# Kernel optimization log

Hardware: AMD Instinct MI355X
Metric: run time of the kernel (lower is better)

## Reference

```python
import jax, jax.numpy as jnp
import numpy as np


def setup_inputs() -> dict:
    key = jax.random.key(0)
    ks = jax.random.split(key, 7)
    B, T, I, H, O = 256, 500, 256, 512, 100
    std = 1.0 / np.sqrt(H)
    u = lambda k, shape: jax.random.uniform(k, shape, jnp.float32, -std, std)
    return {
        "x": jax.random.normal(ks[0], (B, T, I), jnp.float32),
        "Wx": u(ks[1], (4 * H, I)),
        "bx": u(ks[2], (4 * H,)),
        "Wh": u(ks[3], (4 * H, H)),
        "bh": u(ks[4], (4 * H,)),
        "Wfc": jax.random.normal(ks[5], (O, H), jnp.float32) * 0.02,
        "bfc": jnp.zeros((O,), jnp.float32),
    }


def reference(x, Wx, bx, Wh, bh, Wfc, bfc):
    B, T, I = x.shape
    H = Wh.shape[1]
    # Precompute input projections for all timesteps: [T, B, 4H]
    xg = jnp.einsum("bti,gi->tbg", x, Wx) + bx + bh

    def step(carry, xg_t):
        h, c = carry
        gates = xg_t + h @ Wh.T  # [B, 4H]
        i, f, g, o = jnp.split(gates, 4, axis=1)
        i = jax.nn.sigmoid(i)
        f = jax.nn.sigmoid(f)
        g = jnp.tanh(g)
        o = jax.nn.sigmoid(o)
        c = c * f + i * g
        h = o * jnp.tanh(c)
        return (h, c), None

    h0 = jnp.zeros((B, H), x.dtype)
    c0 = jnp.zeros((B, H), x.dtype)
    (hT, _), _ = jax.lax.scan(step, (h0, c0), xg)
    return hT @ Wfc.T + bfc  # [B, O]
```

## Files before the change

### kernel.cpp

```cpp
#include <hip/hip_runtime.h>
#include <hip/hip_bf16.h>

#define B_ 256
#define T_ 500
#define I_ 256
#define H_ 512
#define G_ 2048
#define O_ 100

typedef __attribute__((ext_vector_type(8))) short short8;
typedef __attribute__((ext_vector_type(4))) float f32x4;

#define WHB_OFF 0u
#define WXB_OFF (G_*H_*2u)
#define BSUM_OFF (WXB_OFF + G_*I_*2u)
#define H0_OFF  (BSUM_OFF + G_*4u)
#define H1_OFF  (H0_OFF + B_*H_*2u)
#define C_OFF   (H1_OFF + B_*H_*2u)
#define HT_OFF  (C_OFF + B_*H_*4u)

__device__ __forceinline__ float sigm(float v) { return 1.0f / (1.0f + __expf(-v)); }
__device__ __forceinline__ float tanh_fast(float v) { return 2.0f / (1.0f + __expf(-2.0f * v)) - 1.0f; }

__device__ __forceinline__ short f2bf_s(float f) {
  union { __hip_bfloat16 h; unsigned short u; } cv;
  cv.h = __float2bfloat16(f);
  return (short)cv.u;
}

__global__ void cast_kernel(const float* __restrict__ Wh, const float* __restrict__ Wx,
                            const float* __restrict__ bx, const float* __restrict__ bh,
                            short* __restrict__ Whb, short* __restrict__ Wxb,
                            float* __restrict__ bsum) {
  int idx = blockIdx.x * 256 + threadIdx.x;
  if (idx < G_ * H_) Whb[idx] = f2bf_s(Wh[idx]);
  if (idx < G_ * I_) Wxb[idx] = f2bf_s(Wx[idx]);
  if (idx < G_)      bsum[idx] = bx[idx] + bh[idx];
}

__global__ __launch_bounds__(128)
void lstm_step(const float* __restrict__ x, int t,
               const short* __restrict__ Whb, const short* __restrict__ Wxb,
               const float* __restrict__ bsum,
               const short* __restrict__ h_in,
               unsigned short* __restrict__ h_out,
               float* __restrict__ c,
               float* __restrict__ hT) {
  const int lane = threadIdx.x & 63;
  const int w    = threadIdx.x >> 6;
  const int r    = lane & 15;
  const int ko   = (lane >> 4) << 3;
  const int brow = blockIdx.y * 32 + w * 16;
  const int cbase = blockIdx.x * 16;

  f32x4 acc[4];
  #pragma unroll
  for (int q = 0; q < 4; ++q) { acc[q][0] = 0.f; acc[q][1] = 0.f; acc[q][2] = 0.f; acc[q][3] = 0.f; }

  const short* ha = h_in + (size_t)(brow + r) * H_ + ko;
  #pragma unroll 4
  for (int kk = 0; kk < H_; kk += 32) {
    short8 a = *reinterpret_cast<const short8*>(ha + kk);
    #pragma unroll
    for (int q = 0; q < 4; ++q) {
      const short* bp = Whb + (size_t)(q * H_ + cbase + r) * H_ + kk + ko;
      short8 b = *reinterpret_cast<const short8*>(bp);
      acc[q] = __builtin_amdgcn_mfma_f32_16x16x32_bf16(a, b, acc[q], 0, 0, 0);
    }
  }

  const float* xrow = x + ((size_t)(brow + r) * T_ + t) * I_ + ko;
  #pragma unroll 2
  for (int kk = 0; kk < I_; kk += 32) {
    float4 x0 = *reinterpret_cast<const float4*>(xrow + kk);
    float4 x1 = *reinterpret_cast<const float4*>(xrow + kk + 4);
    short8 a;
    a[0] = f2bf_s(x0.x); a[1] = f2bf_s(x0.y); a[2] = f2bf_s(x0.z); a[3] = f2bf_s(x0.w);
    a[4] = f2bf_s(x1.x); a[5] = f2bf_s(x1.y); a[6] = f2bf_s(x1.z); a[7] = f2bf_s(x1.w);
    #pragma unroll
    for (int q = 0; q < 4; ++q) {
      const short* bp = Wxb + (size_t)(q * H_ + cbase + r) * I_ + kk + ko;
      short8 b = *reinterpret_cast<const short8*>(bp);
      acc[q] = __builtin_amdgcn_mfma_f32_16x16x32_bf16(a, b, acc[q], 0, 0, 0);
    }
  }

  #pragma unroll
  for (int q = 0; q < 4; ++q) {
    float bb = bsum[q * H_ + cbase + r];
    acc[q][0] += bb; acc[q][1] += bb; acc[q][2] += bb; acc[q][3] += bb;
  }

  const int cell = cbase + r;
  #pragma unroll
  for (int j = 0; j < 4; ++j) {
    const int row = brow + ((lane >> 4) << 2) + j;
    const size_t ci = (size_t)row * H_ + cell;
    float ig = sigm(acc[0][j]);
    float fg = sigm(acc[1][j]);
    float gg = tanh_fast(acc[2][j]);
    float og = sigm(acc[3][j]);
    float cn = c[ci] * fg + ig * gg;
    c[ci] = cn;
    float hn = og * tanh_fast(cn);
    h_out[ci] = (unsigned short)f2bf_s(hn);
    if (hT) hT[ci] = hn;
  }
}

__global__ __launch_bounds__(128)
void fc_kernel(const float* __restrict__ hT, const float* __restrict__ Wfc,
               const float* __restrict__ bfc, float* __restrict__ out) {
  int b = blockIdx.x;
  int o = threadIdx.x;
  if (o >= O_) return;
  const float* hr = hT + (size_t)b * H_;
  const float* wr = Wfc + (size_t)o * H_;
  float s = 0.f;
  #pragma unroll 4
  for (int k = 0; k < H_; k += 4) {
    float4 hv = *reinterpret_cast<const float4*>(hr + k);
    float4 wv = *reinterpret_cast<const float4*>(wr + k);
    s += hv.x * wv.x + hv.y * wv.y + hv.z * wv.z + hv.w * wv.w;
  }
  out[b * O_ + o] = s + bfc[o];
}

extern "C" void kernel_launch(void* const* d_in, const int* in_sizes, int n_in,
                              void* d_out, int out_size, void* d_ws, size_t ws_size,
                              hipStream_t stream) {
  const float* x   = (const float*)d_in[0];
  const float* Wx  = (const float*)d_in[1];
  const float* bx  = (const float*)d_in[2];
  const float* Wh  = (const float*)d_in[3];
  const float* bh  = (const float*)d_in[4];
  const float* Wfc = (const float*)d_in[5];
  const float* bfc = (const float*)d_in[6];
  float* out = (float*)d_out;
  char* ws = (char*)d_ws;

  short* Whb  = (short*)(ws + WHB_OFF);
  short* Wxb  = (short*)(ws + WXB_OFF);
  float* bsum = (float*)(ws + BSUM_OFF);
  short* h0   = (short*)(ws + H0_OFF);
  short* h1   = (short*)(ws + H1_OFF);
  float* cbuf = (float*)(ws + C_OFF);
  float* hT   = (float*)(ws + HT_OFF);

  hipMemsetAsync(ws + H0_OFF, 0, B_ * H_ * 2, stream);
  hipMemsetAsync(ws + C_OFF,  0, B_ * H_ * 4, stream);

  cast_kernel<<<(G_ * H_ + 255) / 256, 256, 0, stream>>>(Wh, Wx, bx, bh, Whb, Wxb, bsum);

  for (int t = 0; t < T_; ++t) {
    const short* hin = (t & 1) ? h1 : h0;
    unsigned short* hout = (unsigned short*)((t & 1) ? h0 : h1);
    lstm_step<<<dim3(32, 8), 128, 0, stream>>>(x, t, Whb, Wxb, bsum, hin, hout, cbuf,
                                               (t == T_ - 1) ? hT : nullptr);
  }

  fc_kernel<<<B_, 128, 0, stream>>>(hT, Wfc, bfc, out);
}
```

Before: 6.285 ms.

## Replace per-timestep launches with persistent cooperative LSTM kernel and group barriers

```diff
diff --git a/kernel.cpp b/kernel.cpp
--- a/kernel.cpp
+++ b/kernel.cpp
@@ -8,24 +8,159 @@
 #define G_ 2048
 #define O_ 100
 
+#define NGRP 8
+#define GRP_BLKS 32
+#define CNT_STRIDE 32
+
 typedef __attribute__((ext_vector_type(8))) short short8;
 typedef __attribute__((ext_vector_type(4))) float f32x4;
 
-#define WHB_OFF 0u
-#define WXB_OFF (G_*H_*2u)
+#define WHB_OFF  0u
+#define WXB_OFF  (G_*H_*2u)
 #define BSUM_OFF (WXB_OFF + G_*I_*2u)
-#define H0_OFF  (BSUM_OFF + G_*4u)
-#define H1_OFF  (H0_OFF + B_*H_*2u)
-#define C_OFF   (H1_OFF + B_*H_*2u)
-#define HT_OFF  (C_OFF + B_*H_*4u)
+#define H0_OFF   (BSUM_OFF + G_*4u)
+#define H1_OFF   (H0_OFF + B_*H_*2u)
+#define C_OFF    (H1_OFF + B_*H_*2u)
+#define HT_OFF   (C_OFF + B_*H_*4u)
+#define CNT_OFF  (HT_OFF + B_*H_*4u)
 
 __device__ __forceinline__ float sigm(float v) { return 1.0f / (1.0f + __expf(-v)); }
 __device__ __forceinline__ float tanh_fast(float v) { return 2.0f / (1.0f + __expf(-2.0f * v)) - 1.0f; }
 
-__device__ __forceinline__ short f2bf_s(float f) {
+__device__ __forceinline__ short f2bf(float f) {
   union { __hip_bfloat16 h; unsigned short u; } cv;
   cv.h = __float2bfloat16(f);
   return (short)cv.u;
+}
+__device__ __forceinline__ short8 cvt8(float4 a, float4 b) {
+  short8 s;
+  s[0]=f2bf(a.x); s[1]=f2bf(a.y); s[2]=f2bf(a.z); s[3]=f2bf(a.w);
+  s[4]=f2bf(b.x); s[5]=f2bf(b.y); s[6]=f2bf(b.z); s[7]=f2bf(b.w);
+  return s;
+}
+
+__global__ __launch_bounds__(128, 1)
+void lstm_persist(const float* __restrict__ x, const float* __restrict__ Wx,
+                  const float* __restrict__ bx, const float* __restrict__ Wh,
+                  const float* __restrict__ bh,
+                  unsigned short* __restrict__ hbuf0, unsigned short* __restrict__ hbuf1,
+                  unsigned int* __restrict__ cnt)
+{
+  __shared__ short whlds[32768];
+  char* ldsb = (char*)whlds;
+
+  const int tid = threadIdx.x;
+  const int l   = tid & 63;
+  const int w   = tid >> 6;
+  const int g   = blockIdx.x & 7;
+  const int cc  = blockIdx.x >> 3;
+  const int rbase = g * 32 + w * 16;
+  const int cbase = cc * 16;
+  const int r   = l & 15;
+  const int u   = l >> 4;
+  const int rx  = (r & 7) << 4;
+
+  {
+    const int gc = tid >> 1;
+    const int kh = (tid & 1) * 256;
+    const int q = gc >> 4, li = gc & 15;
+    const float* src = Wh + ((size_t)(q * H_ + cbase + li)) * H_ + kh;
+    const int rowb = gc * (H_ * 2);
+    const int wxz = (gc & 7) << 4;
+    for (int k = 0; k < 256; k += 8) {
+      float4 f0 = *(const float4*)(src + k);
+      float4 f1 = *(const float4*)(src + k + 4);
+      int byte = (rowb + (kh + k) * 2) ^ wxz;
+      *(short8*)(ldsb + byte) = cvt8(f0, f1);
+    }
+  }
+
+  short8 wxr[4][8];
+  #pragma unroll
+  for (int q = 0; q < 4; ++q)
+    #pragma unroll
+    for (int kc = 0; kc < 8; ++kc) {
+      const float* p = Wx + ((size_t)(q * H_ + cbase + r)) * I_ + kc * 32 + u * 8;
+      wxr[q][kc] = cvt8(*(const float4*)p, *(const float4*)(p + 4));
+    }
+
+  float bsum[4];
+  #pragma unroll
+  for (int q = 0; q < 4; ++q)
+    bsum[q] = bx[q * H_ + cbase + r] + bh[q * H_ + cbase + r];
+
+  float creg[4] = {0.f, 0.f, 0.f, 0.f};
+
+  __syncthreads();
+
+  short8 xf[8];
+  #pragma unroll
+  for (int kc = 0; kc < 8; ++kc) {
+    const float* p = x + ((size_t)(rbase + r) * T_ + 0) * I_ + kc * 32 + u * 8;
+    xf[kc] = cvt8(*(const float4*)p, *(const float4*)(p + 4));
+  }
+
+  unsigned int* mycnt = cnt + g * CNT_STRIDE;
+
+  for (int t = 0; t < T_; ++t) {
+    const unsigned short* hin = (t & 1) ? hbuf1 : hbuf0;
+    unsigned short* hout      = (t & 1) ? hbuf0 : hbuf1;
+
+    f32x4 acc[4];
+    #pragma unroll
+    for (int q = 0; q < 4; ++q) acc[q] = (f32x4){0.f, 0.f, 0.f, 0.f};
+
+    #pragma unroll
+    for (int kc = 0; kc < 8; ++kc)
+      #pragma unroll
+      for (int q = 0; q < 4; ++q)
+        acc[q] = __builtin_amdgcn_mfma_f32_16x16x32_bf16(xf[kc], wxr[q][kc], acc[q], 0, 0, 0);
+
+    if (t > 0) {
+      if (tid == 0) {
+        const unsigned int target = (unsigned int)GRP_BLKS * (unsigned int)t;
+        while (__hip_atomic_load(mycnt, __ATOMIC_RELAXED, __HIP_MEMORY_SCOPE_AGENT) < target)
+          __builtin_amdgcn_s_sleep(1);
+      }
+      __syncthreads();
+      __builtin_amdgcn_fence(__ATOMIC_ACQUIRE, "agent");
+    }
+
+    const unsigned short* hp = hin + (size_t)(rbase + r) * H_ + u * 8;
+    #pragma unroll
+    for (int kc = 0; kc < 16; ++kc) {
+      short8 a = *(const short8*)(hp + kc * 32);
+      #pragma unroll
+      for (int q = 0; q < 4; ++q) {
+        int byte = ((q * 16 + r) * (H_ * 2) + kc * 64 + u * 16) ^ rx;
+        short8 b = *(const short8*)(ldsb + byte);
+        acc[q] = __builtin_amdgcn_mfma_f32_16x16x32_bf16(a, b, acc[q], 0, 0, 0);
+      }
+    }
+
+    #pragma unroll
+    for (int j = 0; j < 4; ++j) {
+      float ig = sigm(acc[0][j] + bsum[0]);
+      float fg = sigm(acc[1][j] + bsum[1]);
+      float gg = tanh_fast(acc[2][j] + bsum[2]);
+      float og = sigm(acc[3][j] + bsum[3]);
+      float cn = creg[j] * fg + ig * gg;
+      creg[j] = cn;
+      float hn = og * tanh_fast(cn);
+      hout[(size_t)(rbase + u * 4 + j) * H_ + cbase + r] = (unsigned short)f2bf(hn);
+    }
+
+    if (t + 1 < T_) {
+      __syncthreads();
+      if (tid == 0)
+        __hip_atomic_fetch_add(mycnt, 1u, __ATOMIC_RELEASE, __HIP_MEMORY_SCOPE_AGENT);
+      #pragma unroll
+      for (int kc = 0; kc < 8; ++kc) {
+        const float* p = x + ((size_t)(rbase + r) * T_ + (t + 1)) * I_ + kc * 32 + u * 8;
+        xf[kc] = cvt8(*(const float4*)p, *(const float4*)(p + 4));
+      }
+    }
+  }
 }
 
 __global__ void cast_kernel(const float* __restrict__ Wh, const float* __restrict__ Wx,
@@ -33,8 +168,8 @@
                             short* __restrict__ Whb, short* __restrict__ Wxb,
                             float* __restrict__ bsum) {
   int idx = blockIdx.x * 256 + threadIdx.x;
-  if (idx < G_ * H_) Whb[idx] = f2bf_s(Wh[idx]);
-  if (idx < G_ * I_) Wxb[idx] = f2bf_s(Wx[idx]);
+  if (idx < G_ * H_) Whb[idx] = f2bf(Wh[idx]);
+  if (idx < G_ * I_) Wxb[idx] = f2bf(Wx[idx]);
   if (idx < G_)      bsum[idx] = bx[idx] + bh[idx];
 }
 
@@ -55,7 +190,7 @@
 
   f32x4 acc[4];
   #pragma unroll
-  for (int q = 0; q < 4; ++q) { acc[q][0] = 0.f; acc[q][1] = 0.f; acc[q][2] = 0.f; acc[q][3] = 0.f; }
+  for (int q = 0; q < 4; ++q) acc[q] = (f32x4){0.f, 0.f, 0.f, 0.f};
 
   const short* ha = h_in + (size_t)(brow + r) * H_ + ko;
   #pragma unroll 4
@@ -74,9 +209,7 @@
   for (int kk = 0; kk < I_; kk += 32) {
     float4 x0 = *reinterpret_cast<const float4*>(xrow + kk);
     float4 x1 = *reinterpret_cast<const float4*>(xrow + kk + 4);
-    short8 a;
-    a[0] = f2bf_s(x0.x); a[1] = f2bf_s(x0.y); a[2] = f2bf_s(x0.z); a[3] = f2bf_s(x0.w);
-    a[4] = f2bf_s(x1.x); a[5] = f2bf_s(x1.y); a[6] = f2bf_s(x1.z); a[7] = f2bf_s(x1.w);
+    short8 a = cvt8(x0, x1);
     #pragma unroll
     for (int q = 0; q < 4; ++q) {
       const short* bp = Wxb + (size_t)(q * H_ + cbase + r) * I_ + kk + ko;
@@ -85,32 +218,26 @@
     }
   }
 
-  #pragma unroll
-  for (int q = 0; q < 4; ++q) {
-    float bb = bsum[q * H_ + cbase + r];
-    acc[q][0] += bb; acc[q][1] += bb; acc[q][2] += bb; acc[q][3] += bb;
-  }
-
   const int cell = cbase + r;
   #pragma unroll
   for (int j = 0; j < 4; ++j) {
     const int row = brow + ((lane >> 4) << 2) + j;
     const size_t ci = (size_t)row * H_ + cell;
-    float ig = sigm(acc[0][j]);
-    float fg = sigm(acc[1][j]);
-    float gg = tanh_fast(acc[2][j]);
-    float og = sigm(acc[3][j]);
+    float ig = sigm(acc[0][j] + bsum[0 * H_ + cell]);
+    float fg = sigm(acc[1][j] + bsum[1 * H_ + cell]);
+    float gg = tanh_fast(acc[2][j] + bsum[2 * H_ + cell]);
+    float og = sigm(acc[3][j] + bsum[3 * H_ + cell]);
     float cn = c[ci] * fg + ig * gg;
     c[ci] = cn;
     float hn = og * tanh_fast(cn);
-    h_out[ci] = (unsigned short)f2bf_s(hn);
+    h_out[ci] = (unsigned short)f2bf(hn);
     if (hT) hT[ci] = hn;
   }
 }
 
 __global__ __launch_bounds__(128)
-void fc_kernel(const float* __restrict__ hT, const float* __restrict__ Wfc,
-               const float* __restrict__ bfc, float* __restrict__ out) {
+void fc_f32(const float* __restrict__ hT, const float* __restrict__ Wfc,
+            const float* __restrict__ bfc, float* __restrict__ out) {
   int b = blockIdx.x;
   int o = threadIdx.x;
   if (o >= O_) return;
@@ -122,6 +249,28 @@
     float4 hv = *reinterpret_cast<const float4*>(hr + k);
     float4 wv = *reinterpret_cast<const float4*>(wr + k);
     s += hv.x * wv.x + hv.y * wv.y + hv.z * wv.z + hv.w * wv.w;
+  }
+  out[b * O_ + o] = s + bfc[o];
+}
+
+__global__ __launch_bounds__(128)
+void fc_bf16(const unsigned short* __restrict__ h, const float* __restrict__ Wfc,
+             const float* __restrict__ bfc, float* __restrict__ out) {
+  int b = blockIdx.x;
+  int o = threadIdx.x;
+  if (o >= O_) return;
+  const unsigned short* hr = h + (size_t)b * H_;
+  const float* wr = Wfc + (size_t)o * H_;
+  float s = 0.f;
+  #pragma unroll 4
+  for (int k = 0; k < H_; k += 8) {
+    short8 hv = *(const short8*)(hr + k);
+    #pragma unroll
+    for (int j = 0; j < 8; ++j) {
+      union { unsigned int uu; float f; } cv;
+      cv.uu = ((unsigned int)(unsigned short)hv[j]) << 16;
+      s += cv.f * wr[k + j];
+    }
   }
   out[b * O_ + o] = s + bfc[o];
 }
@@ -139,25 +288,34 @@
   float* out = (float*)d_out;
   char* ws = (char*)d_ws;
 
-  short* Whb  = (short*)(ws + WHB_OFF);
-  short* Wxb  = (short*)(ws + WXB_OFF);
-  float* bsum = (float*)(ws + BSUM_OFF);
-  short* h0   = (short*)(ws + H0_OFF);
-  short* h1   = (short*)(ws + H1_OFF);
-  float* cbuf = (float*)(ws + C_OFF);
-  float* hT   = (float*)(ws + HT_OFF);
+  unsigned short* h0  = (unsigned short*)(ws + H0_OFF);
+  unsigned short* h1  = (unsigned short*)(ws + H1_OFF);
+  unsigned int*   cnt = (unsigned int*)(ws + CNT_OFF);
 
   hipMemsetAsync(ws + H0_OFF, 0, B_ * H_ * 2, stream);
   hipMemsetAsync(ws + C_OFF,  0, B_ * H_ * 4, stream);
-
-  cast_kernel<<<(G_ * H_ + 255) / 256, 256, 0, stream>>>(Wh, Wx, bx, bh, Whb, Wxb, bsum);
-
-  for (int t = 0; t < T_; ++t) {
-    const short* hin = (t & 1) ? h1 : h0;
-    unsigned short* hout = (unsigned short*)((t & 1) ? h0 : h1);
-    lstm_step<<<dim3(32, 8), 128, 0, stream>>>(x, t, Whb, Wxb, bsum, hin, hout, cbuf,
-                                               (t == T_ - 1) ? hT : nullptr);
-  }
-
-  fc_kernel<<<B_, 128, 0, stream>>>(hT, Wfc, bfc, out);
-}
+  hipMemsetAsync(ws + CNT_OFF, 0, NGRP * CNT_STRIDE * 4, stream);
+
+  void* args[] = {(void*)&x, (void*)&Wx, (void*)&bx, (void*)&Wh, (void*)&bh,
+                  (void*)&h0, (void*)&h1, (void*)&cnt};
+  hipError_t e = hipLaunchCooperativeKernel((const void*)lstm_persist,
+                                            dim3(NGRP * GRP_BLKS), dim3(128), args, 0, stream);
+  if (e == hipSuccess) {
+    fc_bf16<<<dim3(B_), dim3(128), 0, stream>>>(h0, Wfc, bfc, out);
+  } else {
+    (void)hipGetLastError();
+    short* Whb  = (short*)(ws + WHB_OFF);
+    short* Wxb  = (short*)(ws + WXB_OFF);
+    float* bsum = (float*)(ws + BSUM_OFF);
+    float* cbuf = (float*)(ws + C_OFF);
+    float* hT   = (float*)(ws + HT_OFF);
+    cast_kernel<<<(G_ * H_ + 255) / 256, 256, 0, stream>>>(Wh, Wx, bx, bh, Whb, Wxb, bsum);
+    for (int t = 0; t < T_; ++t) {
+      const short* hin = (short*)((t & 1) ? h1 : h0);
+      unsigned short* hout = (t & 1) ? h0 : h1;
+      lstm_step<<<dim3(32, 8), 128, 0, stream>>>(x, t, Whb, Wxb, bsum, hin, hout, cbuf,
+                                                 (t == T_ - 1) ? hT : nullptr);
+    }
+    fc_f32<<<dim3(B_), dim3(128), 0, stream>>>(hT, Wfc, bfc, out);
+  }
+}
```

Result: slower. 8.125 ms (+29.3%).
